# Optimization experiments

Hardware: AMD Instinct MI355X
Metric: run time of the kernel (lower is better)

Reference implementation:

```python
import jax, jax.numpy as jnp
import numpy as np

D_MODEL = 1024
NUM_HEADS = 16
D_HEAD = D_MODEL // NUM_HEADS
LN_EPS = 1e-5
ROPE_BASE = 10000.0


def layer_norm(x, w, b=None, eps=LN_EPS):
    mu = jnp.mean(x, axis=-1, keepdims=True)
    var = jnp.mean(jnp.square(x - mu), axis=-1, keepdims=True)
    y = (x - mu) * jax.lax.rsqrt(var + eps) * w
    return y + b if b is not None else y


def _rotate_half(x):
    x1, x2 = jnp.split(x, 2, axis=-1)
    return jnp.concatenate([-x2, x1], axis=-1)


def apply_rotary(q, k):
    # q, k: [B, S, H, Dh]
    s, dh = q.shape[1], q.shape[-1]
    inv_freq = 1.0 / (ROPE_BASE ** (jnp.arange(0, dh, 2, dtype=jnp.float32) / dh))
    t = jnp.arange(s, dtype=jnp.float32)
    freqs = jnp.outer(t, inv_freq)                      # [S, Dh/2]
    emb = jnp.concatenate([freqs, freqs], axis=-1)      # [S, Dh]
    cos = jnp.cos(emb)[None, :, None, :].astype(q.dtype)
    sin = jnp.sin(emb)[None, :, None, :].astype(q.dtype)
    q_rot = q * cos + _rotate_half(q) * sin
    k_rot = k * cos + _rotate_half(k) * sin
    return q_rot, k_rot


def setup_inputs() -> dict:
    key = jax.random.key(0)
    ks = jax.random.split(key, 8)
    B, L, D = 4, 2048, D_MODEL
    x = jax.random.normal(ks[0], (B, L, D), dtype=jnp.float32)
    sequence_id = jnp.sort(jax.random.randint(ks[1], (B, L), 0, 8), axis=-1).astype(jnp.int64)
    scale = 1.0 / np.sqrt(D)
    return {
        "x": x,
        "sequence_id": sequence_id,
        "ln_w": jnp.ones((D,), jnp.float32),
        "ln_b": jnp.zeros((D,), jnp.float32),
        "w_qkv": jax.random.normal(ks[2], (D, 3 * D), jnp.float32) * scale,
        "q_ln_w": jnp.ones((D,), jnp.float32),
        "k_ln_w": jnp.ones((D,), jnp.float32),
        "w_out": jax.random.normal(ks[3], (D, D), jnp.float32) * scale,
    }


def reference(x, sequence_id, ln_w, ln_b, w_qkv, q_ln_w, k_ln_w, w_out):
    B, L, D = x.shape
    H, Dh = NUM_HEADS, D_HEAD
    # fused LayerNorm + QKV projection
    qkv = layer_norm(x, ln_w, ln_b) @ w_qkv              # [B, L, 3D]
    q, k, v = jnp.split(qkv, 3, axis=-1)
    # qk layernorm (scale only, bias=False)
    q = layer_norm(q, q_ln_w)
    k = layer_norm(k, k_ln_w)
    # split heads and apply rotary
    q = q.reshape(B, L, H, Dh)
    k = k.reshape(B, L, H, Dh)
    q, k = apply_rotary(q, k)
    v = v.reshape(B, L, H, Dh)
    # packed-sequence mask: tokens attend only within same sequence id
    mask = (sequence_id[:, :, None] == sequence_id[:, None, :])[:, None, :, :]  # [B,1,L,L]
    scale = 1.0 / np.sqrt(Dh)
    scores = jnp.einsum("bqhd,bkhd->bhqk", q, k) * scale
    scores = jnp.where(mask, scores, jnp.finfo(scores.dtype).min)
    attn = jax.nn.softmax(scores, axis=-1)
    ctx = jnp.einsum("bhqk,bkhd->bqhd", attn, v).reshape(B, L, D)
    return ctx @ w_out
```

## Files before the change

### kernel.cpp

```cpp
#include <hip/hip_runtime.h>
#include <hip/hip_bf16.h>
#include <cstdint>
#include <cstddef>
#include <type_traits>

#define D_MODEL 1024
#define NH      16
#define DH      64
#define LSEQ    2048
#define BATCH   4
#define NTOK    8192
#define K3      3072

typedef __attribute__((ext_vector_type(8))) short  short8;
typedef __attribute__((ext_vector_type(4))) float  floatx4;

__device__ __forceinline__ unsigned short f2bf_bits(float f) {
  __hip_bfloat16 h = __float2bfloat16(f);
  return __builtin_bit_cast(unsigned short, h);
}
__device__ __forceinline__ float bf2f(unsigned short u) {
  return __bfloat162float(__builtin_bit_cast(__hip_bfloat16, u));
}
__device__ __forceinline__ unsigned int pack_bf16(float lo, float hi) {
  return (unsigned int)f2bf_bits(lo) | ((unsigned int)f2bf_bits(hi) << 16);
}

__device__ __forceinline__ void gld_lds16(const void* g, void* l) {
  __builtin_amdgcn_global_load_lds(
      (const __attribute__((address_space(1))) void*)g,
      (__attribute__((address_space(3))) void*)l,
      16, 0, 0);
}

__global__ __launch_bounds__(256)
void prep_kernel(const float* __restrict__ x, const float* __restrict__ ln_w,
                 const float* __restrict__ ln_b, const float* __restrict__ w_qkv,
                 const float* __restrict__ w_out, const int* __restrict__ sid,
                 __hip_bfloat16* __restrict__ hbuf, __hip_bfloat16* __restrict__ wqkvT,
                 __hip_bfloat16* __restrict__ woutT, int* __restrict__ segstart,
                 int* __restrict__ segend) {
  __shared__ __align__(16) char smem[8448];
  const int blk = blockIdx.x;
  const int tid = threadIdx.x;

  if (blk < 4096) {
    float (*tile)[33] = reinterpret_cast<float(*)[33]>(smem);
    const float* src;  __hip_bfloat16* dst;  int R, C, bx, by;
    if (blk < 3072) { src = w_qkv; dst = wqkvT; R = 1024; C = 3072; bx = blk % 96; by = blk / 96; }
    else            { src = w_out; dst = woutT; R = 1024; C = 1024; bx = (blk - 3072) & 31; by = (blk - 3072) >> 5; }
    const int c0 = bx * 32, r0 = by * 32;
    const int xx = tid & 31, yy = tid >> 5;
    #pragma unroll
    for (int j = 0; j < 32; j += 8)
      tile[yy + j][xx] = src[(size_t)(r0 + yy + j) * C + c0 + xx];
    __syncthreads();
    #pragma unroll
    for (int j = 0; j < 32; j += 8)
      dst[(size_t)(c0 + yy + j) * R + r0 + xx] = __float2bfloat16(tile[xx][yy + j]);
  } else if (blk < 6144) {
    const int lane = tid & 63;
    const int t = (blk - 4096) * 4 + (tid >> 6);
    const float4* xr = reinterpret_cast<const float4*>(x) + (size_t)t * 256;
    float4 v[4];
    float s = 0.f, ss = 0.f;
    #pragma unroll
    for (int i = 0; i < 4; i++) {
      v[i] = xr[lane + i * 64];
      s  += (v[i].x + v[i].y) + (v[i].z + v[i].w);
      ss += (v[i].x*v[i].x + v[i].y*v[i].y) + (v[i].z*v[i].z + v[i].w*v[i].w);
    }
    #pragma unroll
    for (int off = 1; off < 64; off <<= 1) {
      s  += __shfl_xor(s, off);
      ss += __shfl_xor(ss, off);
    }
    const float mu = s * (1.f / 1024);
    const float rs = rsqrtf(ss * (1.f / 1024) - mu * mu + 1e-5f);
    const float4* wr = reinterpret_cast<const float4*>(ln_w);
    const float4* br = reinterpret_cast<const float4*>(ln_b);
    ushort4* hr = reinterpret_cast<ushort4*>(hbuf) + (size_t)t * 256;
    #pragma unroll
    for (int i = 0; i < 4; i++) {
      const float4 wv = wr[lane + i * 64];
      const float4 bv = br[lane + i * 64];
      ushort4 o;
      o.x = f2bf_bits((v[i].x - mu) * rs * wv.x + bv.x);
      o.y = f2bf_bits((v[i].y - mu) * rs * wv.y + bv.y);
      o.z = f2bf_bits((v[i].z - mu) * rs * wv.z + bv.z);
      o.w = f2bf_bits((v[i].w - mu) * rs * wv.w + bv.w);
      hr[lane + i * 64] = o;
    }
  } else {
    int* srow = reinterpret_cast<int*>(smem);
    const int sblk = blk - 6144;
    const int b = sblk >> 3;
    const int* row = sid + (size_t)b * LSEQ;
    #pragma unroll
    for (int i = 0; i < 8; i++) srow[tid + i * 256] = row[tid + i * 256];
    __syncthreads();
    const int l = (sblk & 7) * 256 + tid;
    const int v = srow[l];
    int lo = 0, hi = l;
    while (lo < hi) { int mid = (lo + hi) >> 1; if (srow[mid] < v) lo = mid + 1; else hi = mid; }
    const int i = b * LSEQ + l;
    segstart[i] = lo;
    lo = l + 1; hi = LSEQ;
    while (lo < hi) { int mid = (lo + hi) >> 1; if (srow[mid] <= v) lo = mid + 1; else hi = mid; }
    segend[i] = lo;
  }
}

template <typename OutT>
__global__ __launch_bounds__(256, 4)
void gemm_bt(const __hip_bfloat16* __restrict__ A, const __hip_bfloat16* __restrict__ Bt,
             OutT* __restrict__ C, int M, int N, int K) {
  const int tid  = threadIdx.x;
  const int lane = tid & 63;
  const int wave = tid >> 6;
  const int bm = blockIdx.y * 128;
  const int bn = blockIdx.x * 128;
  const int wm = (wave & 1) * 64;
  const int wn = (wave >> 1) * 64;
  const int quad = lane >> 4;
  const int l16  = lane & 15;

  __shared__ __align__(16) __hip_bfloat16 As[128 * 64];
  __shared__ __align__(16) __hip_bfloat16 Bs[128 * 64];

  floatx4 acc[4][4];
  #pragma unroll
  for (int i = 0; i < 4; i++)
    #pragma unroll
    for (int j = 0; j < 4; j++) {
      floatx4 z = {0.f, 0.f, 0.f, 0.f};
      acc[i][j] = z;
    }

  const int srow = tid >> 3;
  const int sq   = tid & 7;
  const int sc8  = (sq ^ (srow & 7)) * 8;
  const __hip_bfloat16* Ab = A  + (size_t)(bm + srow) * K + sc8;
  const __hip_bfloat16* Bb = Bt + (size_t)(bn + srow) * K + sc8;

  const int axr = l16 & 7;

  for (int k0 = 0; k0 < K; k0 += 64) {
    __syncthreads();
    #pragma unroll
    for (int p = 0; p < 4; p++) {
      gld_lds16(Ab + (size_t)(p * 32) * K + k0, (char*)As + p * 4096 + tid * 16);
      gld_lds16(Bb + (size_t)(p * 32) * K + k0, (char*)Bs + p * 4096 + tid * 16);
    }
    __syncthreads();
    #pragma unroll
    for (int s0 = 0; s0 < 2; s0++) {
      const int qo = ((s0 * 4 + quad) ^ axr) * 8;
      short8 af[4], bfr[4];
      #pragma unroll
      for (int i = 0; i < 4; i++)
        af[i] = *reinterpret_cast<const short8*>(As + (wm + i * 16 + l16) * 64 + qo);
      #pragma unroll
      for (int j = 0; j < 4; j++)
        bfr[j] = *reinterpret_cast<const short8*>(Bs + (wn + j * 16 + l16) * 64 + qo);
      #pragma unroll
      for (int i = 0; i < 4; i++)
        #pragma unroll
        for (int j = 0; j < 4; j++)
          acc[i][j] = __builtin_amdgcn_mfma_f32_16x16x32_bf16(af[i], bfr[j], acc[i][j], 0, 0, 0);
    }
  }

  #pragma unroll
  for (int i = 0; i < 4; i++)
    #pragma unroll
    for (int j = 0; j < 4; j++) {
      const int row0 = bm + wm + i * 16 + quad * 4;
      const int col  = bn + wn + j * 16 + l16;
      #pragma unroll
      for (int r = 0; r < 4; r++) {
        if constexpr (std::is_same<OutT, __hip_bfloat16>::value)
          C[(size_t)(row0 + r) * N + col] = __float2bfloat16(acc[i][j][r]);
        else
          C[(size_t)(row0 + r) * N + col] = acc[i][j][r];
      }
    }
}

__global__ __launch_bounds__(256)
void ropevt_kernel(const unsigned short* __restrict__ qkv, const float* __restrict__ qw,
                   const float* __restrict__ kw, unsigned short* __restrict__ qT,
                   unsigned short* __restrict__ kT, unsigned short* __restrict__ vT) {
  __shared__ __align__(16) unsigned short T[64 * 64];
  const int blk = blockIdx.x;
  const int tid = threadIdx.x;

  if (blk < 2048) {
    const int lane = tid & 63;
    const int t = blk * 4 + (tid >> 6);
    const int b = t >> 11, l = t & 2047;
    const unsigned short* row = qkv + (size_t)t * K3;
    const int hh = lane >> 2;
    const int jb = (lane & 3) * 8;
    const int base = hh * 64 + jb;

    const short8 qa_u = *reinterpret_cast<const short8*>(row + base);
    const short8 qb_u = *reinterpret_cast<const short8*>(row + base + 32);
    const short8 ka_u = *reinterpret_cast<const short8*>(row + 1024 + base);
    const short8 kb_u = *reinterpret_cast<const short8*>(row + 1024 + base + 32);

    float qa[8], qb[8], ka[8], kb[8];
    float s_q = 0.f, ss_q = 0.f, s_k = 0.f, ss_k = 0.f;
    #pragma unroll
    for (int e = 0; e < 8; e++) {
      qa[e] = bf2f((unsigned short)qa_u[e]); qb[e] = bf2f((unsigned short)qb_u[e]);
      ka[e] = bf2f((unsigned short)ka_u[e]); kb[e] = bf2f((unsigned short)kb_u[e]);
      s_q  += qa[e] + qb[e];  ss_q += qa[e]*qa[e] + qb[e]*qb[e];
      s_k  += ka[e] + kb[e];  ss_k += ka[e]*ka[e] + kb[e]*kb[e];
    }
    #pragma unroll
    for (int off = 1; off < 64; off <<= 1) {
      s_q  += __shfl_xor(s_q, off);  ss_q += __shfl_xor(ss_q, off);
      s_k  += __shfl_xor(s_k, off);  ss_k += __shfl_xor(ss_k, off);
    }
    const float qmu = s_q * (1.f/1024);
    const float qrs = rsqrtf(ss_q * (1.f/1024) - qmu*qmu + 1e-5f);
    const float kmu = s_k * (1.f/1024);
    const float krs = rsqrtf(ss_k * (1.f/1024) - kmu*kmu + 1e-5f);

    const int j0 = lane & 31;
    const float invf = __expf(-(float)j0 * 0.28782313662425575f);
    float tsin, tcos;
    sincosf((float)l * invf, &tsin, &tcos);

    const float4 wq0 = *reinterpret_cast<const float4*>(qw + base);
    const float4 wq1 = *reinterpret_cast<const float4*>(qw + base + 4);
    const float4 wq2 = *reinterpret_cast<const float4*>(qw + base + 32);
    const float4 wq3 = *reinterpret_cast<const float4*>(qw + base + 36);
    const float4 wk0 = *reinterpret_cast<const float4*>(kw + base);
    const float4 wk1 = *reinterpret_cast<const float4*>(kw + base + 4);
    const float4 wk2 = *reinterpret_cast<const float4*>(kw + base + 32);
    const float4 wk3 = *reinterpret_cast<const float4*>(kw + base + 36);
    const float wqa[8] = {wq0.x,wq0.y,wq0.z,wq0.w, wq1.x,wq1.y,wq1.z,wq1.w};
    const float wqb[8] = {wq2.x,wq2.y,wq2.z,wq2.w, wq3.x,wq3.y,wq3.z,wq3.w};
    const float wka[8] = {wk0.x,wk0.y,wk0.z,wk0.w, wk1.x,wk1.y,wk1.z,wk1.w};
    const float wkb[8] = {wk2.x,wk2.y,wk2.z,wk2.w, wk3.x,wk3.y,wk3.z,wk3.w};

    short8 oqa, oqb, oka, okb;
    #pragma unroll
    for (int e = 0; e < 8; e++) {
      const int j = jb + e;
      const float c  = __shfl(tcos, j);
      const float sn = __shfl(tsin, j);
      const float qn1 = (qa[e] - qmu) * qrs * wqa[e];
      const float qn2 = (qb[e] - qmu) * qrs * wqb[e];
      const float kn1 = (ka[e] - kmu) * krs * wka[e];
      const float kn2 = (kb[e] - kmu) * krs * wkb[e];
      oqa[e] = (short)f2bf_bits((qn1 * c - qn2 * sn) * 0.125f);
      oqb[e] = (short)f2bf_bits((qn2 * c + qn1 * sn) * 0.125f);
      oka[e] = (short)f2bf_bits(kn1 * c - kn2 * sn);
      okb[e] = (short)f2bf_bits(kn2 * c + kn1 * sn);
    }
    const size_t ob = ((size_t)(b * NH + hh) * LSEQ + l) * DH + jb;
    *reinterpret_cast<short8*>(qT + ob)      = oqa;
    *reinterpret_cast<short8*>(qT + ob + 32) = oqb;
    *reinterpret_cast<short8*>(kT + ob)      = oka;
    *reinterpret_cast<short8*>(kT + ob + 32) = okb;
  } else {
    const int blkv = blk - 2048;
    const int l0 = (blkv & 31) * 64;
    const int bh = blkv >> 5;
    const int b = bh >> 4, h = bh & 15;
    const int sr = tid >> 3, scc = tid & 7;
    const int r1 = sr + 32;
    gld_lds16(qkv + (size_t)(b * LSEQ + l0 + sr) * K3 + 2048 + h * 64 + ((scc ^ ((sr >> 3) & 7)) * 8),
              (char*)T + tid * 16);
    gld_lds16(qkv + (size_t)(b * LSEQ + l0 + r1) * K3 + 2048 + h * 64 + ((scc ^ ((r1 >> 3) & 7)) * 8),
              (char*)T + 4096 + tid * 16);
    __syncthreads();
    #pragma unroll
    for (int it = 0; it < 2; it++) {
      const int cid = tid + it * 256;
      const int dh = cid >> 3, c = (cid & 7) * 8;
      const int sl = (dh >> 3) ^ ((c >> 3) & 7);
      short8 o;
      #pragma unroll
      for (int e = 0; e < 8; e++)
        o[e] = (short)T[(c + e) * 64 + sl * 8 + (dh & 7)];
      *reinterpret_cast<short8*>(vT + ((size_t)bh * DH + dh) * LSEQ + l0 + c) = o;
    }
  }
}

__global__ __launch_bounds__(256)
void attn_mfma(const unsigned short* __restrict__ qT, const unsigned short* __restrict__ kT,
               const unsigned short* __restrict__ vT, const int* __restrict__ segs,
               const int* __restrict__ sege, unsigned short* __restrict__ ctx) {
  const int tid  = threadIdx.x;
  const int lane = tid & 63, w = tid >> 6;
  const int quad = lane >> 4, l16 = lane & 15;
  const int qbase = blockIdx.x * 64;
  const int h = blockIdx.y, b = blockIdx.z;
  const int qy = qbase + w * 16 + l16;
  const size_t bh = (size_t)(b * NH + h);
  const unsigned short* Kg = kT + bh * LSEQ * DH;
  const unsigned short* Vg = vT + bh * DH * LSEQ;

  __shared__ __align__(16) unsigned short Ks[64 * 64];
  __shared__ __align__(16) unsigned short Vs[64 * 64];
  __shared__ __align__(16) unsigned short Ps[4][16 * 72];

  const unsigned short* Qrow = qT + (bh * LSEQ + qy) * DH;
  const short8 qf0 = *reinterpret_cast<const short8*>(Qrow + quad * 8);
  const short8 qf1 = *reinterpret_cast<const short8*>(Qrow + 32 + quad * 8);

  const int st = segs[b * LSEQ + qy];
  const int en = sege[b * LSEQ + qy];
  const unsigned span = (unsigned)(en - st);
  const int kmin = segs[b * LSEQ + qbase] & ~63;
  const int kmax = sege[b * LSEQ + qbase + 63];
  const int wmin = segs[b * LSEQ + qbase + w * 16];
  const int wmax = sege[b * LSEQ + qbase + w * 16 + 15];

  floatx4 acc[4];
  #pragma unroll
  for (int dt = 0; dt < 4; dt++) { floatx4 z = {0.f,0.f,0.f,0.f}; acc[dt] = z; }
  float m = -1e30f, lsum = 0.f;

  const int sr  = tid >> 3, scc = tid & 7;
  const int r1  = sr + 32;
  const int sx0 = (scc ^ ((sr >> 3) & 7)) * 8;
  const int sx1 = (scc ^ ((r1 >> 3) & 7)) * 8;
  const int fx  = l16 >> 3;

  for (int kk = kmin; kk < kmax; kk += 64) {
    __syncthreads();
    gld_lds16(Kg + (size_t)(kk + sr) * DH + sx0, (char*)Ks + tid * 16);
    gld_lds16(Kg + (size_t)(kk + r1) * DH + sx1, (char*)Ks + 4096 + tid * 16);
    gld_lds16(Vg + (size_t)sr * LSEQ + kk + sx0, (char*)Vs + tid * 16);
    gld_lds16(Vg + (size_t)r1 * LSEQ + kk + sx1, (char*)Vs + 4096 + tid * 16);
    __syncthreads();

    if (kk + 64 <= wmin || kk >= wmax) continue;

    floatx4 sc[4];
    #pragma unroll
    for (int t = 0; t < 4; t++) {
      const int row = t * 16 + l16;
      const int kx = (2 * t + fx) & 7;
      const short8 kf0 = *reinterpret_cast<const short8*>(Ks + row * 64 + ((quad ^ kx) * 8));
      const short8 kf1 = *reinterpret_cast<const short8*>(Ks + row * 64 + (((quad + 4) ^ kx) * 8));
      floatx4 z = {0.f,0.f,0.f,0.f};
      sc[t] = __builtin_amdgcn_mfma_f32_16x16x32_bf16(kf0, qf0, z, 0, 0, 0);
      sc[t] = __builtin_amdgcn_mfma_f32_16x16x32_bf16(kf1, qf1, sc[t], 0, 0, 0);
    }

    float vm = -1e30f;
    #pragma unroll
    for (int t = 0; t < 4; t++) {
      const int k0 = kk + t * 16 + quad * 4;
      #pragma unroll
      for (int r = 0; r < 4; r++) {
        const bool ok = (unsigned)(k0 + r - st) < span;
        sc[t][r] = ok ? sc[t][r] : -1e30f;
        vm = fmaxf(vm, sc[t][r]);
      }
    }
    vm = fmaxf(vm, __shfl_xor(vm, 16));
    vm = fmaxf(vm, __shfl_xor(vm, 32));
    const float mn = fmaxf(m, vm);
    const float alpha = __expf(m - mn);
    m = mn;

    float rs = 0.f;
    #pragma unroll
    for (int t = 0; t < 4; t++) {
      float p0 = (sc[t][0] > -1e29f) ? __expf(sc[t][0] - mn) : 0.f;
      float p1 = (sc[t][1] > -1e29f) ? __expf(sc[t][1] - mn) : 0.f;
      float p2 = (sc[t][2] > -1e29f) ? __expf(sc[t][2] - mn) : 0.f;
      float p3 = (sc[t][3] > -1e29f) ? __expf(sc[t][3] - mn) : 0.f;
      rs += (p0 + p1) + (p2 + p3);
      uint2 pk;
      pk.x = pack_bf16(p0, p1);
      pk.y = pack_bf16(p2, p3);
      *reinterpret_cast<uint2*>(&Ps[w][l16 * 72 + t * 16 + quad * 4]) = pk;
    }
    rs += __shfl_xor(rs, 16);
    rs += __shfl_xor(rs, 32);
    lsum = lsum * alpha + rs;

    const short8 pf0 = *reinterpret_cast<const short8*>(&Ps[w][l16 * 72 + quad * 8]);
    const short8 pf1 = *reinterpret_cast<const short8*>(&Ps[w][l16 * 72 + 32 + quad * 8]);

    #pragma unroll
    for (int dt = 0; dt < 4; dt++) {
      #pragma unroll
      for (int r = 0; r < 4; r++) acc[dt][r] *= alpha;
      const int row = dt * 16 + l16;
      const int vx = (2 * dt + fx) & 7;
      const short8 vf0 = *reinterpret_cast<const short8*>(Vs + row * 64 + ((quad ^ vx) * 8));
      const short8 vf1 = *reinterpret_cast<const short8*>(Vs + row * 64 + (((quad + 4) ^ vx) * 8));
      acc[dt] = __builtin_amdgcn_mfma_f32_16x16x32_bf16(vf0, pf0, acc[dt], 0, 0, 0);
      acc[dt] = __builtin_amdgcn_mfma_f32_16x16x32_bf16(vf1, pf1, acc[dt], 0, 0, 0);
    }
  }

  const float inv = (lsum > 0.f) ? 1.f / lsum : 0.f;
  unsigned short* orow = ctx + ((size_t)(b * LSEQ + qy)) * D_MODEL + h * DH;
  #pragma unroll
  for (int dt = 0; dt < 4; dt++) {
    uint2 o;
    o.x = pack_bf16(acc[dt][0] * inv, acc[dt][1] * inv);
    o.y = pack_bf16(acc[dt][2] * inv, acc[dt][3] * inv);
    *reinterpret_cast<uint2*>(orow + dt * 16 + quad * 4) = o;
  }
}

extern "C" void kernel_launch(void* const* d_in, const int* in_sizes, int n_in,
                              void* d_out, int out_size, void* d_ws, size_t ws_size,
                              hipStream_t stream) {
  const float* x      = (const float*)d_in[0];
  const int*   sid    = (const int*)d_in[1];
  const float* ln_w   = (const float*)d_in[2];
  const float* ln_b   = (const float*)d_in[3];
  const float* w_qkv  = (const float*)d_in[4];
  const float* q_ln_w = (const float*)d_in[5];
  const float* k_ln_w = (const float*)d_in[6];
  const float* w_out  = (const float*)d_in[7];
  float* out = (float*)d_out;
  char* ws = (char*)d_ws;

  constexpr size_t OFF_WQKVT = 0;
  constexpr size_t OFF_WOUTT = 6291456;
  constexpr size_t OFF_H     = 8388608;
  constexpr size_t OFF_QKV   = 25165824;
  constexpr size_t OFF_QT    = 75497472;
  constexpr size_t OFF_KT    = 92274688;
  constexpr size_t OFF_VT    = 109051904;
  constexpr size_t OFF_CTX   = 125829120;
  constexpr size_t OFF_SEGS  = 142606336;
  constexpr size_t OFF_SEGE  = 142639104;

  __hip_bfloat16* wqkvT = (__hip_bfloat16*)(ws + OFF_WQKVT);
  __hip_bfloat16* woutT = (__hip_bfloat16*)(ws + OFF_WOUTT);
  __hip_bfloat16* hbuf  = (__hip_bfloat16*)(ws + OFF_H);
  __hip_bfloat16* qkvb  = (__hip_bfloat16*)(ws + OFF_QKV);
  unsigned short* qTb   = (unsigned short*)(ws + OFF_QT);
  unsigned short* kTb   = (unsigned short*)(ws + OFF_KT);
  unsigned short* vTb   = (unsigned short*)(ws + OFF_VT);
  unsigned short* ctx   = (unsigned short*)(ws + OFF_CTX);
  int*            segst = (int*)(ws + OFF_SEGS);
  int*            segen = (int*)(ws + OFF_SEGE);

  prep_kernel<<<6176, 256, 0, stream>>>(x, ln_w, ln_b, w_qkv, w_out, sid,
                                        hbuf, wqkvT, woutT, segst, segen);
  gemm_bt<__hip_bfloat16><<<dim3(K3 / 128, NTOK / 128), 256, 0, stream>>>(
      hbuf, wqkvT, qkvb, NTOK, K3, 1024);
  ropevt_kernel<<<4096, 256, 0, stream>>>((const unsigned short*)qkvb, q_ln_w, k_ln_w,
                                          qTb, kTb, vTb);
  attn_mfma<<<dim3(LSEQ / 64, NH, BATCH), 256, 0, stream>>>(qTb, kTb, vTb, segst, segen, ctx);
  gemm_bt<float><<<dim3(D_MODEL / 128, NTOK / 128), 256, 0, stream>>>(
      (const __hip_bfloat16*)ctx, woutT, out, NTOK, D_MODEL, 1024);
}
```

Before: 248.7 us.

## Process 128 queries per attention block and switch K/V staging to padded LDS

```diff
diff --git a/kernel.cpp b/kernel.cpp
--- a/kernel.cpp
+++ b/kernel.cpp
@@ -112,7 +112,7 @@
 }
 
 template <typename OutT>
-__global__ __launch_bounds__(256, 4)
+__global__ __launch_bounds__(256, 2)
 void gemm_bt(const __hip_bfloat16* __restrict__ A, const __hip_bfloat16* __restrict__ Bt,
              OutT* __restrict__ C, int M, int N, int K) {
   const int tid  = threadIdx.x;
@@ -299,120 +299,150 @@
   const int tid  = threadIdx.x;
   const int lane = tid & 63, w = tid >> 6;
   const int quad = lane >> 4, l16 = lane & 15;
-  const int qbase = blockIdx.x * 64;
+  const int qbase = blockIdx.x * 128;
   const int h = blockIdx.y, b = blockIdx.z;
-  const int qy = qbase + w * 16 + l16;
   const size_t bh = (size_t)(b * NH + h);
   const unsigned short* Kg = kT + bh * LSEQ * DH;
   const unsigned short* Vg = vT + bh * DH * LSEQ;
 
-  __shared__ __align__(16) unsigned short Ks[64 * 64];
-  __shared__ __align__(16) unsigned short Vs[64 * 64];
-  __shared__ __align__(16) unsigned short Ps[4][16 * 72];
-
-  const unsigned short* Qrow = qT + (bh * LSEQ + qy) * DH;
-  const short8 qf0 = *reinterpret_cast<const short8*>(Qrow + quad * 8);
-  const short8 qf1 = *reinterpret_cast<const short8*>(Qrow + 32 + quad * 8);
-
-  const int st = segs[b * LSEQ + qy];
-  const int en = sege[b * LSEQ + qy];
-  const unsigned span = (unsigned)(en - st);
+  __shared__ __align__(16) unsigned short Ks[64 * 72];
+  __shared__ __align__(16) unsigned short Vs[64 * 72];
+  __shared__ __align__(16) unsigned short Ps[4][32 * 72];
+
+  short8 qf[2][2];
+  int st[2], en[2];
+  #pragma unroll
+  for (int g = 0; g < 2; g++) {
+    const int qy = qbase + w * 32 + g * 16 + l16;
+    const unsigned short* Qrow = qT + (bh * LSEQ + qy) * DH;
+    qf[g][0] = *reinterpret_cast<const short8*>(Qrow + quad * 8);
+    qf[g][1] = *reinterpret_cast<const short8*>(Qrow + 32 + quad * 8);
+    st[g] = segs[b * LSEQ + qy];
+    en[g] = sege[b * LSEQ + qy];
+  }
+
   const int kmin = segs[b * LSEQ + qbase] & ~63;
-  const int kmax = sege[b * LSEQ + qbase + 63];
-  const int wmin = segs[b * LSEQ + qbase + w * 16];
-  const int wmax = sege[b * LSEQ + qbase + w * 16 + 15];
-
-  floatx4 acc[4];
-  #pragma unroll
-  for (int dt = 0; dt < 4; dt++) { floatx4 z = {0.f,0.f,0.f,0.f}; acc[dt] = z; }
-  float m = -1e30f, lsum = 0.f;
-
-  const int sr  = tid >> 3, scc = tid & 7;
-  const int r1  = sr + 32;
-  const int sx0 = (scc ^ ((sr >> 3) & 7)) * 8;
-  const int sx1 = (scc ^ ((r1 >> 3) & 7)) * 8;
-  const int fx  = l16 >> 3;
+  const int kmax = sege[b * LSEQ + qbase + 127];
+  const int wmin = segs[b * LSEQ + qbase + w * 32];
+  const int wmax = sege[b * LSEQ + qbase + w * 32 + 31];
+  int gmin[2], gmax[2];
+  #pragma unroll
+  for (int g = 0; g < 2; g++) {
+    gmin[g] = segs[b * LSEQ + qbase + w * 32 + g * 16];
+    gmax[g] = sege[b * LSEQ + qbase + w * 32 + g * 16 + 15];
+  }
+
+  floatx4 acc[2][4];
+  #pragma unroll
+  for (int g = 0; g < 2; g++)
+    #pragma unroll
+    for (int dt = 0; dt < 4; dt++) { floatx4 z = {0.f,0.f,0.f,0.f}; acc[g][dt] = z; }
+  float m[2] = {-1e30f, -1e30f}, lsum[2] = {0.f, 0.f};
+
+  const int r_ = tid >> 3, c_ = (tid & 7) * 8;
 
   for (int kk = kmin; kk < kmax; kk += 64) {
     __syncthreads();
-    gld_lds16(Kg + (size_t)(kk + sr) * DH + sx0, (char*)Ks + tid * 16);
-    gld_lds16(Kg + (size_t)(kk + r1) * DH + sx1, (char*)Ks + 4096 + tid * 16);
-    gld_lds16(Vg + (size_t)sr * LSEQ + kk + sx0, (char*)Vs + tid * 16);
-    gld_lds16(Vg + (size_t)r1 * LSEQ + kk + sx1, (char*)Vs + 4096 + tid * 16);
+    #pragma unroll
+    for (int it = 0; it < 2; it++) {
+      const int r = r_ + it * 32;
+      *reinterpret_cast<short8*>(Ks + r * 72 + c_) =
+          *reinterpret_cast<const short8*>(Kg + (size_t)(kk + r) * DH + c_);
+      *reinterpret_cast<short8*>(Vs + r * 72 + c_) =
+          *reinterpret_cast<const short8*>(Vg + (size_t)r * LSEQ + kk + c_);
+    }
     __syncthreads();
 
     if (kk + 64 <= wmin || kk >= wmax) continue;
 
-    floatx4 sc[4];
-    #pragma unroll
-    for (int t = 0; t < 4; t++) {
-      const int row = t * 16 + l16;
-      const int kx = (2 * t + fx) & 7;
-      const short8 kf0 = *reinterpret_cast<const short8*>(Ks + row * 64 + ((quad ^ kx) * 8));
-      const short8 kf1 = *reinterpret_cast<const short8*>(Ks + row * 64 + (((quad + 4) ^ kx) * 8));
-      floatx4 z = {0.f,0.f,0.f,0.f};
-      sc[t] = __builtin_amdgcn_mfma_f32_16x16x32_bf16(kf0, qf0, z, 0, 0, 0);
-      sc[t] = __builtin_amdgcn_mfma_f32_16x16x32_bf16(kf1, qf1, sc[t], 0, 0, 0);
-    }
-
-    float vm = -1e30f;
-    #pragma unroll
-    for (int t = 0; t < 4; t++) {
-      const int k0 = kk + t * 16 + quad * 4;
-      #pragma unroll
-      for (int r = 0; r < 4; r++) {
-        const bool ok = (unsigned)(k0 + r - st) < span;
-        sc[t][r] = ok ? sc[t][r] : -1e30f;
-        vm = fmaxf(vm, sc[t][r]);
+    float alpha[2];
+    bool act[2];
+    #pragma unroll
+    for (int g = 0; g < 2; g++) {
+      act[g] = !(kk + 64 <= gmin[g] || kk >= gmax[g]);
+      alpha[g] = 1.f;
+      if (!act[g]) continue;
+
+      floatx4 sc[4];
+      #pragma unroll
+      for (int t = 0; t < 4; t++) {
+        const short8 kf0 = *reinterpret_cast<const short8*>(Ks + (t * 16 + l16) * 72 + quad * 8);
+        const short8 kf1 = *reinterpret_cast<const short8*>(Ks + (t * 16 + l16) * 72 + 32 + quad * 8);
+        floatx4 z = {0.f,0.f,0.f,0.f};
+        sc[t] = __builtin_amdgcn_mfma_f32_16x16x32_bf16(kf0, qf[g][0], z, 0, 0, 0);
+        sc[t] = __builtin_amdgcn_mfma_f32_16x16x32_bf16(kf1, qf[g][1], sc[t], 0, 0, 0);
       }
-    }
-    vm = fmaxf(vm, __shfl_xor(vm, 16));
-    vm = fmaxf(vm, __shfl_xor(vm, 32));
-    const float mn = fmaxf(m, vm);
-    const float alpha = __expf(m - mn);
-    m = mn;
-
-    float rs = 0.f;
-    #pragma unroll
-    for (int t = 0; t < 4; t++) {
-      float p0 = (sc[t][0] > -1e29f) ? __expf(sc[t][0] - mn) : 0.f;
-      float p1 = (sc[t][1] > -1e29f) ? __expf(sc[t][1] - mn) : 0.f;
-      float p2 = (sc[t][2] > -1e29f) ? __expf(sc[t][2] - mn) : 0.f;
-      float p3 = (sc[t][3] > -1e29f) ? __expf(sc[t][3] - mn) : 0.f;
-      rs += (p0 + p1) + (p2 + p3);
-      uint2 pk;
-      pk.x = pack_bf16(p0, p1);
-      pk.y = pack_bf16(p2, p3);
-      *reinterpret_cast<uint2*>(&Ps[w][l16 * 72 + t * 16 + quad * 4]) = pk;
-    }
-    rs += __shfl_xor(rs, 16);
-    rs += __shfl_xor(rs, 32);
-    lsum = lsum * alpha + rs;
-
-    const short8 pf0 = *reinterpret_cast<const short8*>(&Ps[w][l16 * 72 + quad * 8]);
-    const short8 pf1 = *reinterpret_cast<const short8*>(&Ps[w][l16 * 72 + 32 + quad * 8]);
-
+
+      const unsigned span = (unsigned)(en[g] - st[g]);
+      float vm = -1e30f;
+      #pragma unroll
+      for (int t = 0; t < 4; t++) {
+        const int k0 = kk + t * 16 + quad * 4;
+        #pragma unroll
+        for (int r = 0; r < 4; r++) {
+          const bool ok = (unsigned)(k0 + r - st[g]) < span;
+          sc[t][r] = ok ? sc[t][r] : -1e30f;
+          vm = fmaxf(vm, sc[t][r]);
+        }
+      }
+      vm = fmaxf(vm, __shfl_xor(vm, 16));
+      vm = fmaxf(vm, __shfl_xor(vm, 32));
+      const float mn = fmaxf(m[g], vm);
+      alpha[g] = __expf(m[g] - mn);
+      m[g] = mn;
+
+      float rs = 0.f;
+      #pragma unroll
+      for (int t = 0; t < 4; t++) {
+        float p0 = (sc[t][0] > -1e29f) ? __expf(sc[t][0] - mn) : 0.f;
+        float p1 = (sc[t][1] > -1e29f) ? __expf(sc[t][1] - mn) : 0.f;
+        float p2 = (sc[t][2] > -1e29f) ? __expf(sc[t][2] - mn) : 0.f;
+        float p3 = (sc[t][3] > -1e29f) ? __expf(sc[t][3] - mn) : 0.f;
+        rs += (p0 + p1) + (p2 + p3);
+        uint2 pk;
+        pk.x = pack_bf16(p0, p1);
+        pk.y = pack_bf16(p2, p3);
+        *reinterpret_cast<uint2*>(&Ps[w][(g * 16 + l16) * 72 + t * 16 + quad * 4]) = pk;
+      }
+      rs += __shfl_xor(rs, 16);
+      rs += __shfl_xor(rs, 32);
+      lsum[g] = lsum[g] * alpha[g] + rs;
+    }
+
+    short8 pf[2][2];
+    #pragma unroll
+    for (int g = 0; g < 2; g++) {
+      if (!act[g]) continue;
+      pf[g][0] = *reinterpret_cast<const short8*>(&Ps[w][(g * 16 + l16) * 72 + quad * 8]);
+      pf[g][1] = *reinterpret_cast<const short8*>(&Ps[w][(g * 16 + l16) * 72 + 32 + quad * 8]);
+    }
     #pragma unroll
     for (int dt = 0; dt < 4; dt++) {
-      #pragma unroll
-      for (int r = 0; r < 4; r++) acc[dt][r] *= alpha;
-      const int row = dt * 16 + l16;
-      const int vx = (2 * dt + fx) & 7;
-      const short8 vf0 = *reinterpret_cast<const short8*>(Vs + row * 64 + ((quad ^ vx) * 8));
-      const short8 vf1 = *reinterpret_cast<const short8*>(Vs + row * 64 + (((quad + 4) ^ vx) * 8));
-      acc[dt] = __builtin_amdgcn_mfma_f32_16x16x32_bf16(vf0, pf0, acc[dt], 0, 0, 0);
-      acc[dt] = __builtin_amdgcn_mfma_f32_16x16x32_bf16(vf1, pf1, acc[dt], 0, 0, 0);
-    }
-  }
-
-  const float inv = (lsum > 0.f) ? 1.f / lsum : 0.f;
-  unsigned short* orow = ctx + ((size_t)(b * LSEQ + qy)) * D_MODEL + h * DH;
-  #pragma unroll
-  for (int dt = 0; dt < 4; dt++) {
-    uint2 o;
-    o.x = pack_bf16(acc[dt][0] * inv, acc[dt][1] * inv);
-    o.y = pack_bf16(acc[dt][2] * inv, acc[dt][3] * inv);
-    *reinterpret_cast<uint2*>(orow + dt * 16 + quad * 4) = o;
+      const short8 vf0 = *reinterpret_cast<const short8*>(Vs + (dt * 16 + l16) * 72 + quad * 8);
+      const short8 vf1 = *reinterpret_cast<const short8*>(Vs + (dt * 16 + l16) * 72 + 32 + quad * 8);
+      #pragma unroll
+      for (int g = 0; g < 2; g++) {
+        if (!act[g]) continue;
+        #pragma unroll
+        for (int r = 0; r < 4; r++) acc[g][dt][r] *= alpha[g];
+        acc[g][dt] = __builtin_amdgcn_mfma_f32_16x16x32_bf16(vf0, pf[g][0], acc[g][dt], 0, 0, 0);
+        acc[g][dt] = __builtin_amdgcn_mfma_f32_16x16x32_bf16(vf1, pf[g][1], acc[g][dt], 0, 0, 0);
+      }
+    }
+  }
+
+  #pragma unroll
+  for (int g = 0; g < 2; g++) {
+    const float inv = (lsum[g] > 0.f) ? 1.f / lsum[g] : 0.f;
+    const int qy = qbase + w * 32 + g * 16 + l16;
+    unsigned short* orow = ctx + ((size_t)(b * LSEQ + qy)) * D_MODEL + h * DH;
+    #pragma unroll
+    for (int dt = 0; dt < 4; dt++) {
+      uint2 o;
+      o.x = pack_bf16(acc[g][dt][0] * inv, acc[g][dt][1] * inv);
+      o.y = pack_bf16(acc[g][dt][2] * inv, acc[g][dt][3] * inv);
+      *reinterpret_cast<uint2*>(orow + dt * 16 + quad * 4) = o;
+    }
   }
 }
 
@@ -458,7 +488,7 @@
       hbuf, wqkvT, qkvb, NTOK, K3, 1024);
   ropevt_kernel<<<4096, 256, 0, stream>>>((const unsigned short*)qkvb, q_ln_w, k_ln_w,
                                           qTb, kTb, vTb);
-  attn_mfma<<<dim3(LSEQ / 64, NH, BATCH), 256, 0, stream>>>(qTb, kTb, vTb, segst, segen, ctx);
+  attn_mfma<<<dim3(LSEQ / 128, NH, BATCH), 256, 0, stream>>>(qTb, kTb, vTb, segst, segen, ctx);
   gemm_bt<float><<<dim3(D_MODEL / 128, NTOK / 128), 256, 0, stream>>>(
       (const __hip_bfloat16*)ctx, woutT, out, NTOK, D_MODEL, 1024);
 }
```

New measurement: 247.9 us. About the same (-0.3%).
